# Performance work log

Measured on AMD Instinct MI355X. Metric: run time of the kernel, lower is better.

## Reference

```python
import jax, jax.numpy as jnp
import numpy as np

BS = 64          # BSR block size
B, D_IN, H, D_OUT = 4096, 1024, 4096, 1024
DENSITY = 0.5    # fraction of nonzero 64x64 blocks in fc2


def setup_inputs() -> dict:
    key = jax.random.key(0)
    ks = jax.random.split(key, 4)
    x = jax.random.normal(ks[0], (B, D_IN), jnp.float32)
    w1 = jax.random.normal(ks[1], (H, D_IN), jnp.float32) * (1.0 / np.sqrt(D_IN))
    b1 = jnp.zeros((H,), jnp.float32)
    w3 = jax.random.normal(ks[2], (D_OUT, H), jnp.float32) * (1.0 / np.sqrt(H))
    b3 = jnp.zeros((D_OUT,), jnp.float32)
    # Build BSR structure for fc2 weight [H, H]: block grid is (H//BS, H//BS)
    nbr, nbc = H // BS, H // BS
    rng = np.random.default_rng(0)
    mask = rng.random((nbr, nbc)) < DENSITY
    mask[:, 0] = True  # ensure each block row has at least one block
    crow = np.concatenate([[0], np.cumsum(mask.sum(axis=1))]).astype(np.int32)
    col = np.concatenate([np.nonzero(mask[r])[0] for r in range(nbr)]).astype(np.int32)
    nnzb = int(col.shape[0])
    values = jax.random.normal(ks[3], (nnzb, BS, BS), jnp.float32) * (1.0 / np.sqrt(H))
    return {
        "x": x, "w1": w1, "b1": b1,
        "values": values, "w3": w3, "b3": b3,
        "crow_indices": jnp.asarray(crow),
        "col_indices": jnp.asarray(col),
    }


def bsr_linear(x, crow, col, values, n_block_rows):
    """y = x @ W.T where W [out, in] is BSR with blocks values[nnzb, bs, bs]."""
    bsz = x.shape[0]
    bs = values.shape[1]
    nnzb = col.shape[0]
    # block row index of each nonzero block, from CSR row pointers
    block_row = jnp.searchsorted(crow, jnp.arange(nnzb, dtype=crow.dtype), side='right') - 1
    xb = x.reshape(bsz, -1, bs)            # [B, n_block_cols, bs]
    gath = xb[:, col]                      # [B, nnzb, bs] irregular gather
    # per-block contribution: block is W[row_blk, col_blk] of shape [bs_out, bs_in]
    contrib = jnp.einsum('bni,noi->nbo', gath, values)  # [nnzb, B, bs]
    yb = jax.ops.segment_sum(contrib, block_row, num_segments=n_block_rows)  # [nbr, B, bs]
    return yb.transpose(1, 0, 2).reshape(bsz, n_block_rows * bs)


def reference(x, w1, b1, values, w3, b3, crow_indices, col_indices):
    # Flatten is a no-op for 2D input
    h = jax.nn.relu(x @ w1.T + b1)                                   # fc1 + ReLU
    h = jax.nn.relu(bsr_linear(h, crow_indices, col_indices, values, H // BS))  # BSR fc2 + ReLU
    return h @ w3.T + b3                                             # fc3
```

## Files before the change

kernel.cpp:

```cpp
#include <hip/hip_runtime.h>
#include <hip/hip_bf16.h>
#include <stdint.h>


typedef __attribute__((ext_vector_type(4))) float f32x4;
typedef __attribute__((ext_vector_type(8))) __bf16 bf16x8;

#define DEV static __device__ __forceinline__

DEV ushort f2bf(float f) {
  union { float f; uint32_t u; } v; v.f = f;
  uint32_t r = v.u + 0x7fffu + ((v.u >> 16) & 1u);
  return (ushort)(r >> 16);
}

DEV void gld_lds16(const void* g, void* l) {
  __builtin_amdgcn_global_load_lds(
      (const __attribute__((address_space(1))) void*)g,
      (__attribute__((address_space(3))) void*)l, 16, 0, 0);
}

__global__ void cvt4_kernel(const float* __restrict__ s0, ushort* __restrict__ d0, int n0,
                            const float* __restrict__ s1, ushort* __restrict__ d1, int n1,
                            const float* __restrict__ s2, ushort* __restrict__ d2, int n2,
                            const float* __restrict__ s3, ushort* __restrict__ d3, int n3) {
  const int total = (n0 + n1 + n2 + n3) >> 2;
  for (int idx = blockIdx.x * blockDim.x + threadIdx.x; idx < total;
       idx += gridDim.x * blockDim.x) {
    int i = idx * 4;
    const float* s; ushort* d;
    if (i < n0)               { s = s0; d = d0; }
    else if ((i -= n0) < n1)  { s = s1; d = d1; }
    else if ((i -= n1) < n2)  { s = s2; d = d2; }
    else                      { i -= n2; s = s3; d = d3; }
    float4 v = *(const float4*)(s + i);
    ushort4 o;
    o.x = f2bf(v.x); o.y = f2bf(v.y); o.z = f2bf(v.z); o.w = f2bf(v.w);
    *(ushort4*)(d + i) = o;
  }
}

__global__ void combine_kernel(const float* __restrict__ p0, const float* __restrict__ p1,
                               const float* __restrict__ bias, float* __restrict__ out,
                               int total, int ncols) {
  int i = (blockIdx.x * blockDim.x + threadIdx.x) * 4;
  if (i >= total) return;
  float4 a = *(const float4*)(p0 + i);
  float4 b = *(const float4*)(p1 + i);
  const float4 bv = *(const float4*)(bias + (i & (ncols - 1)));
  a.x += b.x + bv.x; a.y += b.y + bv.y; a.z += b.z + bv.z; a.w += b.w + bv.w;
  *(float4*)(out + i) = a;
}

template <bool RELU, bool OUT_BF16>
__global__ __launch_bounds__(256)
void gemm_nt(const ushort* __restrict__ A, const ushort* __restrict__ W,
             const float* __restrict__ bias, void* __restrict__ Cv,
             int K, int lda, int ldw, int ldc, int ntx, int nty) {
  const int bid = blockIdx.x;
  const int xcd = bid & 7;
  const int j = bid >> 3;
  const int xgrp = ntx >> 3;
  const int bx = xcd + 8 * (j % xgrp);
  const int by = j / xgrp;
  const int i0 = by * 128, j0 = bx * 128;

  __shared__ ushort As[128 * 64];
  __shared__ ushort Ws[128 * 64];
  const int tid = threadIdx.x;
  const int wid = tid >> 6, lane = tid & 63;
  const int wm = wid >> 1, wn = wid & 1;
  f32x4 acc[4][4] = {};

  const int lrow = lane >> 3;
  const int lcol = (lane & 7) * 16;

  for (int k0 = 0; k0 < K; k0 += 64) {
#pragma unroll
    for (int i = 0; i < 4; ++i) {
      int ch = wid * 4 + i;
      int row = ch * 8 + lrow;
      const char* ga = (const char*)A + ((size_t)(i0 + row) * lda + k0) * 2 + lcol;
      gld_lds16(ga, (char*)As + ch * 1024);
      const char* gw = (const char*)W + ((size_t)(j0 + row) * ldw + k0) * 2 + lcol;
      gld_lds16(gw, (char*)Ws + ch * 1024);
    }
    __syncthreads();
#pragma unroll
    for (int kk = 0; kk < 64; kk += 32) {
      const int cl = lane & 15;
      const int kg = kk + (lane >> 4) * 8;
      bf16x8 a[4], b[4];
#pragma unroll
      for (int m = 0; m < 4; ++m)
        a[m] = *(const bf16x8*)&As[(wm * 64 + m * 16 + cl) * 64 + kg];
#pragma unroll
      for (int n = 0; n < 4; ++n)
        b[n] = *(const bf16x8*)&Ws[(wn * 64 + n * 16 + cl) * 64 + kg];
#pragma unroll
      for (int m = 0; m < 4; ++m)
#pragma unroll
        for (int n = 0; n < 4; ++n)
          acc[m][n] = __builtin_amdgcn_mfma_f32_16x16x32_bf16(a[m], b[n], acc[m][n], 0, 0, 0);
    }
    __syncthreads();
  }

  const int cl = lane & 15, r4 = (lane >> 4) * 4;
#pragma unroll
  for (int n = 0; n < 4; ++n) {
    int col = j0 + wn * 64 + n * 16 + cl;
    float bv = bias ? bias[col] : 0.0f;
#pragma unroll
    for (int m = 0; m < 4; ++m) {
      int rowb = i0 + wm * 64 + m * 16 + r4;
#pragma unroll
      for (int r = 0; r < 4; ++r) {
        float v = acc[m][n][r] + bv;
        if (RELU) v = fmaxf(v, 0.0f);
        if (OUT_BF16)
          ((ushort*)Cv)[(size_t)(rowb + r) * ldc + col] = f2bf(v);
        else
          ((float*)Cv)[(size_t)(rowb + r) * ldc + col] = v;
      }
    }
  }
}

__global__ __launch_bounds__(256)
void gemm_nt_sk(const ushort* __restrict__ A, const ushort* __restrict__ W,
                float* __restrict__ P0, float* __restrict__ P1,
                int Khalf, int lda, int ldw, int ldc) {
  const int bid = blockIdx.x;
  const int combo = bid & 15;
  const int kidx = combo >> 3;
  const int bx = combo & 7;
  const int by = bid >> 4;
  const ushort* Ao = A + (size_t)kidx * Khalf;
  const ushort* Wo = W + (size_t)kidx * Khalf;
  float* P = kidx ? P1 : P0;

  __shared__ ushort As[128 * 64];
  __shared__ ushort Ws[128 * 64];
  const int tid = threadIdx.x;
  const int wid = tid >> 6, lane = tid & 63;
  const int wm = wid >> 1, wn = wid & 1;
  const int i0 = by * 128, j0 = bx * 128;
  f32x4 acc[4][4] = {};

  const int lrow = lane >> 3;
  const int lcol = (lane & 7) * 16;

  for (int k0 = 0; k0 < Khalf; k0 += 64) {
#pragma unroll
    for (int i = 0; i < 4; ++i) {
      int ch = wid * 4 + i;
      int row = ch * 8 + lrow;
      const char* ga = (const char*)Ao + ((size_t)(i0 + row) * lda + k0) * 2 + lcol;
      gld_lds16(ga, (char*)As + ch * 1024);
      const char* gw = (const char*)Wo + ((size_t)(j0 + row) * ldw + k0) * 2 + lcol;
      gld_lds16(gw, (char*)Ws + ch * 1024);
    }
    __syncthreads();
#pragma unroll
    for (int kk = 0; kk < 64; kk += 32) {
      const int cl = lane & 15;
      const int kg = kk + (lane >> 4) * 8;
      bf16x8 a[4], b[4];
#pragma unroll
      for (int m = 0; m < 4; ++m)
        a[m] = *(const bf16x8*)&As[(wm * 64 + m * 16 + cl) * 64 + kg];
#pragma unroll
      for (int n = 0; n < 4; ++n)
        b[n] = *(const bf16x8*)&Ws[(wn * 64 + n * 16 + cl) * 64 + kg];
#pragma unroll
      for (int m = 0; m < 4; ++m)
#pragma unroll
        for (int n = 0; n < 4; ++n)
          acc[m][n] = __builtin_amdgcn_mfma_f32_16x16x32_bf16(a[m], b[n], acc[m][n], 0, 0, 0);
    }
    __syncthreads();
  }

  const int cl = lane & 15, r4 = (lane >> 4) * 4;
#pragma unroll
  for (int n = 0; n < 4; ++n) {
    int col = j0 + wn * 64 + n * 16 + cl;
#pragma unroll
    for (int m = 0; m < 4; ++m) {
      int rowb = i0 + wm * 64 + m * 16 + r4;
#pragma unroll
      for (int r = 0; r < 4; ++r)
        P[(size_t)(rowb + r) * ldc + col] = acc[m][n][r];
    }
  }
}

__global__ __launch_bounds__(256)
void bsr_gemm(const ushort* __restrict__ A, const ushort* __restrict__ V,
              const int* __restrict__ crow, const int* __restrict__ colind,
              ushort* __restrict__ C, int Hdim) {
  __shared__ ushort As[2][128 * 64];
  __shared__ ushort Vs[2][64 * 64];
  const int tid = threadIdx.x;
  const int wid = tid >> 6, lane = tid & 63;

  const int bid = blockIdx.x;
  const int xcd = bid & 7;
  const int j = bid >> 3;
  const int tile = xcd + 8 * (j & 3);
  const int br = j >> 2;
  const int i0 = tile * 128;

  f32x4 acc[2][4] = {};
  const int n0 = crow[br], n1 = crow[br + 1];

  const int lr = lane >> 3;
  const int gsw = ((lane & 7) ^ lr) * 16;

  const char* gb[6];
#pragma unroll
  for (int i = 0; i < 6; ++i) {
    int ch = wid * 6 + i;
    if (ch < 16) gb[i] = (const char*)A + (size_t)(i0 + ch * 8 + lr) * Hdim * 2 + gsw;
    else         gb[i] = (const char*)V + (size_t)((ch - 16) * 8 + lr) * 128 + gsw;
  }

  auto stage = [&](int buf, int n) {
    const int c = colind[n];
    const size_t aoff = (size_t)c << 7;
    const size_t voff = (size_t)n << 13;
#pragma unroll
    for (int i = 0; i < 6; ++i) {
      int ch = wid * 6 + i;
      if (ch < 16) gld_lds16(gb[i] + aoff, (char*)As[buf] + ch * 1024);
      else         gld_lds16(gb[i] + voff, (char*)Vs[buf] + (ch - 16) * 1024);
    }
  };

  auto compute = [&](int buf) {
#pragma unroll
    for (int kk = 0; kk < 64; kk += 32) {
      const int cl = lane & 15;
      const int kg = kk + (lane >> 4) * 8;
      const int kx = kg ^ ((cl & 7) << 3);
      bf16x8 a[2], b[4];
#pragma unroll
      for (int m = 0; m < 2; ++m)
        a[m] = *(const bf16x8*)&As[buf][(wid * 32 + m * 16 + cl) * 64 + kx];
#pragma unroll
      for (int nn = 0; nn < 4; ++nn)
        b[nn] = *(const bf16x8*)&Vs[buf][(nn * 16 + cl) * 64 + kx];
      __builtin_amdgcn_s_setprio(1);
#pragma unroll
      for (int m = 0; m < 2; ++m)
#pragma unroll
        for (int nn = 0; nn < 4; ++nn)
          acc[m][nn] = __builtin_amdgcn_mfma_f32_16x16x32_bf16(a[m], b[nn], acc[m][nn], 0, 0, 0);
      __builtin_amdgcn_s_setprio(0);
    }
  };

  int cur = 0;
  stage(0, n0);
  __syncthreads();
  for (int n = n0; n < n1; ++n) {
    if (n + 1 < n1) stage(cur ^ 1, n + 1);
    compute(cur);
    __syncthreads();
    cur ^= 1;
  }

  const int cl = lane & 15, r4 = (lane >> 4) * 4;
#pragma unroll
  for (int nn = 0; nn < 4; ++nn) {
    int col = br * 64 + nn * 16 + cl;
#pragma unroll
    for (int m = 0; m < 2; ++m) {
      int rowb = i0 + wid * 32 + m * 16 + r4;
#pragma unroll
      for (int r = 0; r < 4; ++r) {
        float v = fmaxf(acc[m][nn][r], 0.0f);
        C[(size_t)(rowb + r) * Hdim + col] = f2bf(v);
      }
    }
  }
}

extern "C" void kernel_launch(void* const* d_in, const int* in_sizes, int n_in,
                              void* d_out, int out_size, void* d_ws, size_t ws_size,
                              hipStream_t stream) {
  const float* x    = (const float*)d_in[0];
  const float* w1   = (const float*)d_in[1];
  const float* b1   = (const float*)d_in[2];
  const float* vals = (const float*)d_in[3];
  const float* w3   = (const float*)d_in[4];
  const float* b3   = (const float*)d_in[5];
  const int* crow   = (const int*)d_in[6];
  const int* colind = (const int*)d_in[7];

  const int Bb = 4096, Din = 1024, H = 4096, Dout = 1024;
  const int nnzb = in_sizes[7];

  char* ws = (char*)d_ws;
  size_t off = 0;
  ushort* xb  = (ushort*)(ws + off); off += (size_t)Bb * Din * 2;
  ushort* w1b = (ushort*)(ws + off); off += (size_t)H * Din * 2;
  ushort* w3b = (ushort*)(ws + off); off += (size_t)Dout * H * 2;
  ushort* vb  = (ushort*)(ws + off); off += (size_t)nnzb * 64 * 64 * 2;
  ushort* h1b = (ushort*)(ws + off); off += (size_t)Bb * H * 2;
  ushort* h2b = (ushort*)(ws + off); off += (size_t)Bb * H * 2;
  float* p0 = (float*)(ws + off); off += (size_t)Bb * Dout * 4;
  float* p1 = (float*)(ws + off); off += (size_t)Bb * Dout * 4;
  const bool can_splitk = (off <= ws_size);

  hipLaunchKernelGGL(cvt4_kernel, dim3(2048), dim3(256), 0, stream,
                     x,    xb,  Bb * Din,
                     w1,   w1b, H * Din,
                     w3,   w3b, Dout * H,
                     vals, vb,  nnzb * 4096);

  hipLaunchKernelGGL((gemm_nt<true, true>), dim3((H / 128) * (Bb / 128)), dim3(256), 0, stream,
                     xb, w1b, b1, (void*)h1b, Din, Din, Din, H, H / 128, Bb / 128);
  hipLaunchKernelGGL(bsr_gemm, dim3((Bb / 128) * (H / 64)), dim3(256), 0, stream,
                     h1b, vb, crow, colind, h2b, H);
  if (can_splitk) {
    hipLaunchKernelGGL(gemm_nt_sk, dim3(2 * (Dout / 128) * (Bb / 128)), dim3(256), 0, stream,
                       h2b, w3b, p0, p1, H / 2, H, H, Dout);
    int total = Bb * Dout;
    hipLaunchKernelGGL(combine_kernel, dim3((total / 4 + 255) / 256), dim3(256), 0, stream,
                       p0, p1, b3, (float*)d_out, total, Dout);
  } else {
    hipLaunchKernelGGL((gemm_nt<false, false>), dim3((Dout / 128) * (Bb / 128)), dim3(256), 0, stream,
                       h2b, w3b, b3, d_out, H, H, H, Dout, Dout / 128, Bb / 128);
  }
}
```

Before: 230.4 us.

## Replace split-K fc3 with 128x64-tile double-buffered GEMM fusing bias

The fc3 GEMM no longer splits K into two partial-sum buffers followed by a combine kernel. It now uses 128x64 output tiles, giving 512 blocks over the full K. The new kernel double-buffers LDS loads and XOR-swizzles the LDS layout to avoid bank conflicts. It raises MFMA priority via setprio and adds the bias in the epilogue. This removes the fp32 partial writes, their re-reads and one launch, at the cost of lower per-tile reuse from the narrower N tile.

```diff
diff --git a/kernel.cpp b/kernel.cpp
--- a/kernel.cpp
+++ b/kernel.cpp
@@ -40,18 +40,6 @@
   }
 }
 
-__global__ void combine_kernel(const float* __restrict__ p0, const float* __restrict__ p1,
-                               const float* __restrict__ bias, float* __restrict__ out,
-                               int total, int ncols) {
-  int i = (blockIdx.x * blockDim.x + threadIdx.x) * 4;
-  if (i >= total) return;
-  float4 a = *(const float4*)(p0 + i);
-  float4 b = *(const float4*)(p1 + i);
-  const float4 bv = *(const float4*)(bias + (i & (ncols - 1)));
-  a.x += b.x + bv.x; a.y += b.y + bv.y; a.z += b.z + bv.z; a.w += b.w + bv.w;
-  *(float4*)(out + i) = a;
-}
-
 template <bool RELU, bool OUT_BF16>
 __global__ __launch_bounds__(256)
 void gemm_nt(const ushort* __restrict__ A, const ushort* __restrict__ W,
@@ -128,70 +116,87 @@
 }
 
 __global__ __launch_bounds__(256)
-void gemm_nt_sk(const ushort* __restrict__ A, const ushort* __restrict__ W,
-                float* __restrict__ P0, float* __restrict__ P1,
-                int Khalf, int lda, int ldw, int ldc) {
-  const int bid = blockIdx.x;
-  const int combo = bid & 15;
-  const int kidx = combo >> 3;
-  const int bx = combo & 7;
-  const int by = bid >> 4;
-  const ushort* Ao = A + (size_t)kidx * Khalf;
-  const ushort* Wo = W + (size_t)kidx * Khalf;
-  float* P = kidx ? P1 : P0;
-
-  __shared__ ushort As[128 * 64];
-  __shared__ ushort Ws[128 * 64];
+void gemm_n64(const ushort* __restrict__ A, const ushort* __restrict__ W,
+              const float* __restrict__ bias, float* __restrict__ Cout,
+              int K, int lda, int ldw, int ldc) {
+  __shared__ ushort As[2][128 * 64];
+  __shared__ ushort Ws[2][64 * 64];
   const int tid = threadIdx.x;
   const int wid = tid >> 6, lane = tid & 63;
-  const int wm = wid >> 1, wn = wid & 1;
-  const int i0 = by * 128, j0 = bx * 128;
-  f32x4 acc[4][4] = {};
-
-  const int lrow = lane >> 3;
-  const int lcol = (lane & 7) * 16;
-
-  for (int k0 = 0; k0 < Khalf; k0 += 64) {
-#pragma unroll
-    for (int i = 0; i < 4; ++i) {
-      int ch = wid * 4 + i;
-      int row = ch * 8 + lrow;
-      const char* ga = (const char*)Ao + ((size_t)(i0 + row) * lda + k0) * 2 + lcol;
-      gld_lds16(ga, (char*)As + ch * 1024);
-      const char* gw = (const char*)Wo + ((size_t)(j0 + row) * ldw + k0) * 2 + lcol;
-      gld_lds16(gw, (char*)Ws + ch * 1024);
-    }
-    __syncthreads();
+
+  const int bid = blockIdx.x;
+  const int bx = (bid & 7) + 8 * ((bid >> 3) & 1);
+  const int by = bid >> 4;
+  const int i0 = by * 128, j0 = bx * 64;
+
+  f32x4 acc[2][4] = {};
+  const int nt = K >> 6;
+
+  const int lr = lane >> 3;
+  const int gsw = ((lane & 7) ^ lr) * 16;
+
+  const char* gb[6];
+#pragma unroll
+  for (int i = 0; i < 6; ++i) {
+    int ch = wid * 6 + i;
+    if (ch < 16) gb[i] = (const char*)A + (size_t)(i0 + ch * 8 + lr) * lda * 2 + gsw;
+    else         gb[i] = (const char*)W + (size_t)(j0 + (ch - 16) * 8 + lr) * ldw * 2 + gsw;
+  }
+
+  auto stage = [&](int buf, int s) {
+    const size_t koff = (size_t)s << 7;
+#pragma unroll
+    for (int i = 0; i < 6; ++i) {
+      int ch = wid * 6 + i;
+      if (ch < 16) gld_lds16(gb[i] + koff, (char*)As[buf] + ch * 1024);
+      else         gld_lds16(gb[i] + koff, (char*)Ws[buf] + (ch - 16) * 1024);
+    }
+  };
+
+  auto compute = [&](int buf) {
 #pragma unroll
     for (int kk = 0; kk < 64; kk += 32) {
       const int cl = lane & 15;
       const int kg = kk + (lane >> 4) * 8;
-      bf16x8 a[4], b[4];
-#pragma unroll
-      for (int m = 0; m < 4; ++m)
-        a[m] = *(const bf16x8*)&As[(wm * 64 + m * 16 + cl) * 64 + kg];
-#pragma unroll
-      for (int n = 0; n < 4; ++n)
-        b[n] = *(const bf16x8*)&Ws[(wn * 64 + n * 16 + cl) * 64 + kg];
-#pragma unroll
-      for (int m = 0; m < 4; ++m)
-#pragma unroll
-        for (int n = 0; n < 4; ++n)
-          acc[m][n] = __builtin_amdgcn_mfma_f32_16x16x32_bf16(a[m], b[n], acc[m][n], 0, 0, 0);
-    }
+      const int kx = kg ^ ((cl & 7) << 3);
+      bf16x8 a[2], b[4];
+#pragma unroll
+      for (int m = 0; m < 2; ++m)
+        a[m] = *(const bf16x8*)&As[buf][(wid * 32 + m * 16 + cl) * 64 + kx];
+#pragma unroll
+      for (int nn = 0; nn < 4; ++nn)
+        b[nn] = *(const bf16x8*)&Ws[buf][(nn * 16 + cl) * 64 + kx];
+      __builtin_amdgcn_s_setprio(1);
+#pragma unroll
+      for (int m = 0; m < 2; ++m)
+#pragma unroll
+        for (int nn = 0; nn < 4; ++nn)
+          acc[m][nn] = __builtin_amdgcn_mfma_f32_16x16x32_bf16(a[m], b[nn], acc[m][nn], 0, 0, 0);
+      __builtin_amdgcn_s_setprio(0);
+    }
+  };
+
+  int cur = 0;
+  stage(0, 0);
+  __syncthreads();
+  for (int s = 0; s < nt; ++s) {
+    if (s + 1 < nt) stage(cur ^ 1, s + 1);
+    compute(cur);
     __syncthreads();
+    cur ^= 1;
   }
 
   const int cl = lane & 15, r4 = (lane >> 4) * 4;
 #pragma unroll
-  for (int n = 0; n < 4; ++n) {
-    int col = j0 + wn * 64 + n * 16 + cl;
-#pragma unroll
-    for (int m = 0; m < 4; ++m) {
-      int rowb = i0 + wm * 64 + m * 16 + r4;
+  for (int nn = 0; nn < 4; ++nn) {
+    int col = j0 + nn * 16 + cl;
+    const float bv = bias[col];
+#pragma unroll
+    for (int m = 0; m < 2; ++m) {
+      int rowb = i0 + wid * 32 + m * 16 + r4;
 #pragma unroll
       for (int r = 0; r < 4; ++r)
-        P[(size_t)(rowb + r) * ldc + col] = acc[m][n][r];
+        Cout[(size_t)(rowb + r) * ldc + col] = acc[m][nn][r] + bv;
     }
   }
 }
@@ -310,9 +315,6 @@
   ushort* vb  = (ushort*)(ws + off); off += (size_t)nnzb * 64 * 64 * 2;
   ushort* h1b = (ushort*)(ws + off); off += (size_t)Bb * H * 2;
   ushort* h2b = (ushort*)(ws + off); off += (size_t)Bb * H * 2;
-  float* p0 = (float*)(ws + off); off += (size_t)Bb * Dout * 4;
-  float* p1 = (float*)(ws + off); off += (size_t)Bb * Dout * 4;
-  const bool can_splitk = (off <= ws_size);
 
   hipLaunchKernelGGL(cvt4_kernel, dim3(2048), dim3(256), 0, stream,
                      x,    xb,  Bb * Din,
@@ -324,14 +326,6 @@
                      xb, w1b, b1, (void*)h1b, Din, Din, Din, H, H / 128, Bb / 128);
   hipLaunchKernelGGL(bsr_gemm, dim3((Bb / 128) * (H / 64)), dim3(256), 0, stream,
                      h1b, vb, crow, colind, h2b, H);
-  if (can_splitk) {
-    hipLaunchKernelGGL(gemm_nt_sk, dim3(2 * (Dout / 128) * (Bb / 128)), dim3(256), 0, stream,
-                       h2b, w3b, p0, p1, H / 2, H, H, Dout);
-    int total = Bb * Dout;
-    hipLaunchKernelGGL(combine_kernel, dim3((total / 4 + 255) / 256), dim3(256), 0, stream,
-                       p0, p1, b3, (float*)d_out, total, Dout);
-  } else {
-    hipLaunchKernelGGL((gemm_nt<false, false>), dim3((Dout / 128) * (Bb / 128)), dim3(256), 0, stream,
-                       h2b, w3b, b3, d_out, H, H, H, Dout, Dout / 128, Bb / 128);
-  }
-}
+  hipLaunchKernelGGL(gemm_n64, dim3((Dout / 64) * (Bb / 128)), dim3(256), 0, stream,
+                     h2b, w3b, b3, (float*)d_out, H, H, H, Dout);
+}
```

Measured after the change: 217.2 us (median of 2 runs). 5.7% less time.
